# Performance work log

Hardware: AMD Instinct MI355X
Metric: run time of the kernel (lower is better)

Reference implementation:

```python
import jax, jax.numpy as jnp
from jax import lax
import numpy as np


def _conv(x, w):
    # x: [B,Cin,H,W], w: [Cout,Cin,kh,kw] -> [B,Cout,H,W], SAME padding
    return lax.conv_general_dilated(x, w, (1, 1), 'SAME')


def setup_inputs() -> dict:
    key = jax.random.key(0)
    ks = jax.random.split(key, 16)
    B, Hh, W = 8, 256, 256
    inputs = jax.random.normal(ks[0], (B, Hh, W), jnp.float32)
    H0 = jax.random.normal(ks[1], (B, Hh, W), jnp.float32)
    C0 = jax.random.normal(ks[2], (B, 2, Hh, W), jnp.float32)
    # learned scalars: c2 ~ U(0,1), sf ~ N(0, 0.01) shifted away from 0 (it is a divisor)
    c2 = jax.random.uniform(ks[3], (1,), jnp.float32, 0.0, 1.0)
    sf = 0.01 * jax.random.normal(ks[4], (1,), jnp.float32) + 0.02
    # RedNet (assumed small conv encoder-decoder): 1->32->64->32->1, 3x3 SAME, ReLU
    w1 = 0.1 * jax.random.normal(ks[5], (32, 1, 3, 3), jnp.float32)
    b1 = jnp.zeros((32,), jnp.float32)
    w2 = 0.1 * jax.random.normal(ks[6], (64, 32, 3, 3), jnp.float32)
    b2 = jnp.zeros((64,), jnp.float32)
    w3 = 0.1 * jax.random.normal(ks[7], (32, 64, 3, 3), jnp.float32)
    b3 = jnp.zeros((32,), jnp.float32)
    w4 = 0.1 * jax.random.normal(ks[8], (1, 32, 3, 3), jnp.float32)
    b4 = jnp.zeros((1,), jnp.float32)
    return dict(inputs=inputs, H0=H0, C0=C0, c2=c2, sf=sf,
                w1=w1, b1=b1, w2=w2, b2=b2, w3=w3, b3=b3, w4=w4, b4=b4)


def reference(inputs, H0, C0, c2, sf, w1, b1, w2, b2, w3, b3, w4, b4):
    # Fixed 5-point Laplacian stencil (non-trainable in the original module)
    lap_k = jnp.array([[0., 1., 0.], [1., -4., 1.], [0., 1., 0.]],
                      dtype=inputs.dtype)[None, None]  # [1,1,3,3]

    # torch chain: C' = permute/matmul(Wcc^T)/permute + wcu*U
    #   reduces exactly to: C'[:,0] = inputs, C'[:,1] = C_old[:,0]
    C_new = jnp.stack([inputs, C0[:, 0]], axis=1)  # [B,2,H,W]

    V = inputs - H0  # [B,H,W]

    # H = whc . C' = 2*C'[:,0] - C'[:,1] = 2*inputs - C_old[:,0]
    lap = _conv(inputs[:, None], lap_k)[:, 0]  # [B,H,W]
    H = 2.0 * inputs - C0[:, 0] + c2 * lap

    # RedNet on scaled residual V
    h = (V / sf)[:, None]  # [B,1,H,W]
    h = jax.nn.relu(_conv(h, w1) + b1[None, :, None, None])
    h = jax.nn.relu(_conv(h, w2) + b2[None, :, None, None])
    h = jax.nn.relu(_conv(h, w3) + b3[None, :, None, None])
    V_hat = (_conv(h, w4) + b4[None, :, None, None])[:, 0] * sf  # [B,H,W]

    outputs = H + V_hat
    return (outputs, H, C_new, V, V_hat)
```

## Files before the change

kernel.cpp:

```cpp
#include <hip/hip_runtime.h>

#define PLANE 65536
#define WIDTH 256
#define PADW 258
#define PADPLANE 66564

typedef __bf16 v8bf __attribute__((ext_vector_type(8)));
typedef float  v4f  __attribute__((ext_vector_type(4)));

typedef const __attribute__((address_space(1))) unsigned int* gas_ptr;
typedef __attribute__((address_space(3))) unsigned int* las_ptr;

__device__ __forceinline__ void gl_lds(const void* g, void* l) {
  __builtin_amdgcn_global_load_lds((gas_ptr)g, (las_ptr)l, 16, 0, 0);
}

__device__ __forceinline__ int swz(int c) {
  return (c & ~7) | ((c & 7) ^ ((c >> 3) & 7));
}

__device__ __forceinline__ unsigned int pack2(float a, float b) {
  __bf16 ba = (__bf16)a, bb = (__bf16)b;
  unsigned short sa = __builtin_bit_cast(unsigned short, ba);
  unsigned short sb = __builtin_bit_cast(unsigned short, bb);
  return (unsigned int)sa | ((unsigned int)sb << 16);
}

#define WT_N 37440
#define ZR_N (8 * 1028 * 64)
__global__ __launch_bounds__(256) void wz_k(
    const float* __restrict__ w1, const float* __restrict__ w2,
    const float* __restrict__ w3, const float* __restrict__ w4,
    float* __restrict__ w1t, __bf16* __restrict__ B2t,
    __bf16* __restrict__ B3t, float* __restrict__ w4t,
    __bf16* __restrict__ a1, __bf16* __restrict__ a2,
    __bf16* __restrict__ a3)
{
  int t = blockIdx.x * 256 + threadIdx.x;
  if (t < WT_N) {
    if (t < 288) {
      int tap = t >> 5, cout = t & 31;
      w1t[t] = w1[cout * 9 + tap];
    }
    int t2 = t - 288;
    if (t2 >= 0 && t2 < 18432) {
      int cout = t2 / 288, k = t2 % 288;
      int tap = k / 32, cin = k % 32;
      B2t[t2] = (__bf16)w2[cout * 288 + cin * 9 + tap];
    }
    int t3 = t - (288 + 18432);
    if (t3 >= 0 && t3 < 18432) {
      int cout = t3 / 576, k = t3 % 576;
      int tap = k / 64, cin = k % 64;
      B3t[t3] = (__bf16)w3[cout * 576 + cin * 9 + tap];
    }
    int t4 = t - (288 + 18432 + 18432);
    if (t4 >= 0 && t4 < 288) {
      int tap = t4 >> 5, cin = t4 & 31;
      w4t[t4] = w4[cin * 9 + tap];
    }
    return;
  }
  int idx = t - WT_N;
  if (idx >= ZR_N) return;
  unsigned int* p; int C2;
  const int R1 = 8 * 1028 * 16, R2 = 8 * 1028 * 32;
  if (idx < R1)           { p = (unsigned int*)a1; C2 = 16; }
  else if (idx < R1 + R2) { p = (unsigned int*)a2; C2 = 32; idx -= R1; }
  else                    { p = (unsigned int*)a3; C2 = 16; idx -= R1 + R2; }
  int ch = idx % C2;
  int pr = idx / C2;
  int b = pr / 1028, r = pr % 1028;
  int y, x;
  if      (r < 258) { y = 0;           x = r; }
  else if (r < 516) { y = 257;         x = r - 258; }
  else if (r < 772) { y = r - 516 + 1; x = 0; }
  else              { y = r - 772 + 1; x = 257; }
  p[((size_t)b * PADPLANE + y * PADW + x) * C2 + ch] = 0;
}

__global__ __launch_bounds__(256) void prepconv1_k(
    const float* __restrict__ inputs, const float* __restrict__ H0,
    const float* __restrict__ C0, const float* __restrict__ c2p,
    const float* __restrict__ sfp, const float* __restrict__ w1t,
    const float* __restrict__ b1, float* __restrict__ dout,
    __bf16* __restrict__ act1)
{
  const int x = threadIdx.x, y = blockIdx.x, b = blockIdx.y;
  const int p = b * PLANE + y * WIDTH + x;
  const float c2 = c2p[0], sf = sfp[0], rsf = 1.0f / sf;

  float iv[3][3], hv[3][3];
  #pragma unroll
  for (int dy = 0; dy < 3; dy++) {
    int yy = y + dy - 1;
    #pragma unroll
    for (int dx = 0; dx < 3; dx++) {
      int xx = x + dx - 1;
      bool ok = (yy >= 0 && yy < 256 && xx >= 0 && xx < 256);
      int pn = p + (dy - 1) * WIDTH + (dx - 1);
      iv[dy][dx] = ok ? inputs[pn] : 0.f;
      hv[dy][dx] = ok ? H0[pn]     : 0.f;
    }
  }
  const float in = iv[1][1], h0 = hv[1][1];
  const float c0a = C0[b * 131072 + y * WIDTH + x];
  float lap = iv[0][1] + iv[2][1] + iv[1][0] + iv[1][2] - 4.f * in;
  float Hv = 2.f * in - c0a + c2 * lap;
  float V  = in - h0;
  dout[524288 + p]  = Hv;
  dout[2097152 + p] = V;
  dout[1048576 + b * 131072 + y * WIDTH + x]         = in;
  dout[1048576 + b * 131072 + 65536 + y * WIDTH + x] = c0a;

  float acc[32];
  #pragma unroll
  for (int i = 0; i < 32; i++) acc[i] = b1[i];
  #pragma unroll
  for (int tap = 0; tap < 9; tap++) {
    float v = (iv[tap / 3][tap % 3] - hv[tap / 3][tap % 3]) * rsf;
    const float* wp = w1t + tap * 32;
    #pragma unroll
    for (int i = 0; i < 32; i++) acc[i] = fmaf(wp[i], v, acc[i]);
  }
  unsigned int u[16];
  #pragma unroll
  for (int j = 0; j < 16; j++)
    u[j] = pack2(fmaxf(acc[2*j], 0.f), fmaxf(acc[2*j+1], 0.f));
  size_t pa = ((size_t)b * PADPLANE + (y+1) * PADW + (x+1)) * 32;
  uint4* op = reinterpret_cast<uint4*>(act1 + pa);
  #pragma unroll
  for (int j = 0; j < 4; j++)
    op[j] = make_uint4(u[4*j], u[4*j+1], u[4*j+2], u[4*j+3]);
}

#define C2ROWB 8320
template<int ROWS>
__global__ __launch_bounds__(256, 2) void conv2_k(
    const __bf16* __restrict__ in, const __bf16* __restrict__ Bt,
    const float* __restrict__ bias, __bf16* __restrict__ out)
{
  const int lane = threadIdx.x & 63, wave = threadIdx.x >> 6;
  const int l15 = lane & 15, q = lane >> 4;
  const int y0 = blockIdx.x * ROWS, xt = blockIdx.y, b = blockIdx.z;
  const int x0 = xt * 128;
  __shared__ __align__(16) char smem[3 * C2ROWB];
  const __bf16* plane = in + (size_t)b * PADPLANE * 32;

  auto stage = [&](int pr, char* lrow) {
    const char* g = (const char*)(plane + ((size_t)pr * PADW + x0) * 32);
    const int base = wave * 130;
    #pragma unroll
    for (int j = 0; j < 2; j++) {
      int c = base + j * 64 + lane;
      gl_lds(g + (size_t)swz(c) * 16, lrow + (base + j * 64) * 16);
    }
    if (lane < 2) {
      int c = base + 128 + lane;
      gl_lds(g + (size_t)swz(c) * 16, lrow + (base + 128) * 16);
    }
  };

  v8bf breg[9][4];
  #pragma unroll
  for (int tap = 0; tap < 9; tap++)
    #pragma unroll
    for (int nt = 0; nt < 4; nt++)
      breg[tap][nt] = *(const v8bf*)(Bt + (size_t)(nt * 16 + l15) * 288
                                        + tap * 32 + q * 8);
  float bv[4];
  #pragma unroll
  for (int nt = 0; nt < 4; nt++) bv[nt] = bias[nt * 16 + l15];

  #pragma unroll
  for (int r = 0; r < 3; r++) stage(y0 + r, smem + r * C2ROWB);
  __syncthreads();

  for (int i = 0; i < ROWS; i++) {
    v4f acc[2][4];
    #pragma unroll
    for (int mt = 0; mt < 2; mt++)
      #pragma unroll
      for (int nt = 0; nt < 4; nt++)
        acc[mt][nt] = (v4f){bv[nt], bv[nt], bv[nt], bv[nt]};

    #pragma unroll
    for (int tap = 0; tap < 9; tap++) {
      const int dy = tap / 3, dx = tap % 3;
      const char* srow = smem + ((i + dy) % 3) * C2ROWB;
      v8bf af[2];
      #pragma unroll
      for (int mt = 0; mt < 2; mt++) {
        int P = wave * 32 + mt * 16 + l15 + dx;
        af[mt] = *(const v8bf*)(srow + (size_t)swz(P * 4 + q) * 16);
      }
      #pragma unroll
      for (int mt = 0; mt < 2; mt++)
        #pragma unroll
        for (int nt = 0; nt < 4; nt++)
          acc[mt][nt] = __builtin_amdgcn_mfma_f32_16x16x32_bf16(
              af[mt], breg[tap][nt], acc[mt][nt], 0, 0, 0);
    }
    {
      size_t rb = ((size_t)b * PADPLANE + (size_t)(y0 + i + 1) * PADW
                   + x0 + 1) * 64;
      #pragma unroll
      for (int mt = 0; mt < 2; mt++) {
        #pragma unroll
        for (int r = 0; r < 4; r++) {
          size_t pa = rb + (size_t)(wave * 32 + mt * 16 + q * 4 + r) * 64;
          #pragma unroll
          for (int nt = 0; nt < 4; nt++)
            out[pa + nt * 16 + l15] = (__bf16)fmaxf(acc[mt][nt][r], 0.f);
        }
      }
    }
    __syncthreads();
    if (i + 3 < ROWS + 2)
      stage(y0 + i + 3, smem + (i % 3) * C2ROWB);
    __syncthreads();
  }
}

#define C3ROWB 16640
template<int ROWS>
__global__ __launch_bounds__(256, 2) void conv3_k(
    const __bf16* __restrict__ in, const __bf16* __restrict__ Bt,
    const float* __restrict__ bias, __bf16* __restrict__ out)
{
  const int lane = threadIdx.x & 63, wave = threadIdx.x >> 6;
  const int l15 = lane & 15, q = lane >> 4;
  const int y0 = blockIdx.x * ROWS, xt = blockIdx.y, b = blockIdx.z;
  const int x0 = xt * 128;
  __shared__ __align__(16) char smem[4 * C3ROWB];
  const __bf16* plane = in + (size_t)b * PADPLANE * 64;

  auto stage = [&](int pr, char* lrow) {
    const char* g = (const char*)(plane + ((size_t)pr * PADW + x0) * 64);
    const int base = wave * 260;
    #pragma unroll
    for (int j = 0; j < 4; j++) {
      int c = base + j * 64 + lane;
      gl_lds(g + (size_t)swz(c) * 16, lrow + (base + j * 64) * 16);
    }
    if (lane < 4) {
      int c = base + 256 + lane;
      gl_lds(g + (size_t)swz(c) * 16, lrow + (base + 256) * 16);
    }
  };

  v8bf breg[9][2][2];
  #pragma unroll
  for (int tap = 0; tap < 9; tap++)
    #pragma unroll
    for (int kb = 0; kb < 2; kb++)
      #pragma unroll
      for (int nt = 0; nt < 2; nt++)
        breg[tap][kb][nt] = *(const v8bf*)(Bt + (size_t)(nt * 16 + l15) * 576
                                              + tap * 64 + kb * 32 + q * 8);
  float bv[2] = {bias[l15], bias[16 + l15]};

  #pragma unroll
  for (int r = 0; r < 4; r++) stage(y0 + r, smem + r * C3ROWB);
  __syncthreads();

  for (int ps = 0; ps < ROWS / 2; ps++) {
    v4f acc[2][2][2];
    #pragma unroll
    for (int rr = 0; rr < 2; rr++)
      #pragma unroll
      for (int mt = 0; mt < 2; mt++)
        #pragma unroll
        for (int nt = 0; nt < 2; nt++)
          acc[rr][mt][nt] = (v4f){bv[nt], bv[nt], bv[nt], bv[nt]};

    #pragma unroll
    for (int t = 0; t < 4; t++) {
      const char* srow = smem + ((2 * ps + t) & 3) * C3ROWB;
      #pragma unroll
      for (int dx = 0; dx < 3; dx++) {
        #pragma unroll
        for (int kb = 0; kb < 2; kb++) {
          v8bf af[2];
          #pragma unroll
          for (int mt = 0; mt < 2; mt++) {
            int P = wave * 32 + mt * 16 + l15 + dx;
            af[mt] = *(const v8bf*)(srow + (size_t)swz(P * 8 + kb * 4 + q) * 16);
          }
          #pragma unroll
          for (int mt = 0; mt < 2; mt++)
            #pragma unroll
            for (int nt = 0; nt < 2; nt++) {
              if (t <= 2)
                acc[0][mt][nt] = __builtin_amdgcn_mfma_f32_16x16x32_bf16(
                    af[mt], breg[t * 3 + dx][kb][nt], acc[0][mt][nt], 0, 0, 0);
              if (t >= 1)
                acc[1][mt][nt] = __builtin_amdgcn_mfma_f32_16x16x32_bf16(
                    af[mt], breg[(t - 1) * 3 + dx][kb][nt], acc[1][mt][nt],
                    0, 0, 0);
            }
        }
      }
    }
    {
      #pragma unroll
      for (int rr = 0; rr < 2; rr++) {
        size_t rb = ((size_t)b * PADPLANE
                     + (size_t)(y0 + 2 * ps + rr + 1) * PADW + x0 + 1) * 32;
        #pragma unroll
        for (int mt = 0; mt < 2; mt++) {
          #pragma unroll
          for (int r = 0; r < 4; r++) {
            size_t pa = rb + (size_t)(wave * 32 + mt * 16 + q * 4 + r) * 32;
            #pragma unroll
            for (int nt = 0; nt < 2; nt++)
              out[pa + nt * 16 + l15] = (__bf16)fmaxf(acc[rr][mt][nt][r], 0.f);
          }
        }
      }
    }
    __syncthreads();
    if (ps + 1 < ROWS / 2) {
      stage(y0 + 2 * ps + 4, smem + ((2 * ps) & 3) * C3ROWB);
      stage(y0 + 2 * ps + 5, smem + ((2 * ps + 1) & 3) * C3ROWB);
    }
    __syncthreads();
  }
}

__global__ __launch_bounds__(256) void conv4_k(
    const __bf16* __restrict__ act3, const float* __restrict__ w4t,
    const float* __restrict__ b4, const float* __restrict__ sfp,
    float* __restrict__ dout)
{
  const int x = threadIdx.x, y0 = blockIdx.x * 2, b = blockIdx.y;
  const float b4v = b4[0], sf = sfp[0];
  const uint4* base = (const uint4*)(act3 + (size_t)b * PADPLANE * 32);
  float acc0 = b4v, acc1 = b4v;

  #pragma unroll
  for (int t = 0; t < 4; t++) {
    const uint4* rp = base + ((size_t)(y0 + t) * PADW + x) * 4;
    uint4 L[12];
    #pragma unroll
    for (int j = 0; j < 12; j++) L[j] = rp[j];
    #pragma unroll
    for (int j = 0; j < 12; j++) {
      const int dx = j >> 2, c0 = (j & 3) * 8;
      unsigned int uu[4] = {L[j].x, L[j].y, L[j].z, L[j].w};
      float f[8];
      #pragma unroll
      for (int k = 0; k < 4; k++) {
        f[2*k]   = __builtin_bit_cast(float, uu[k] << 16);
        f[2*k+1] = __builtin_bit_cast(float, uu[k] & 0xFFFF0000u);
      }
      if (t <= 2) {
        const float* wp = w4t + (t * 3 + dx) * 32 + c0;
        #pragma unroll
        for (int k = 0; k < 8; k++) acc0 = fmaf(wp[k], f[k], acc0);
      }
      if (t >= 1) {
        const float* wp = w4t + ((t - 1) * 3 + dx) * 32 + c0;
        #pragma unroll
        for (int k = 0; k < 8; k++) acc1 = fmaf(wp[k], f[k], acc1);
      }
    }
  }
  size_t p0 = ((size_t)b << 16) + (size_t)y0 * WIDTH + x;
  float vh0 = acc0 * sf, vh1 = acc1 * sf;
  dout[p0]                   = dout[524288 + p0] + vh0;
  dout[2621440 + p0]         = vh0;
  dout[p0 + WIDTH]           = dout[524288 + p0 + WIDTH] + vh1;
  dout[2621440 + p0 + WIDTH] = vh1;
}

extern "C" void kernel_launch(void* const* d_in, const int* in_sizes, int n_in,
                              void* d_out, int out_size, void* d_ws, size_t ws_size,
                              hipStream_t stream) {
  const float* inputs = (const float*)d_in[0];
  const float* H0     = (const float*)d_in[1];
  const float* C0     = (const float*)d_in[2];
  const float* c2     = (const float*)d_in[3];
  const float* sf     = (const float*)d_in[4];
  const float* w1     = (const float*)d_in[5];
  const float* b1     = (const float*)d_in[6];
  const float* w2     = (const float*)d_in[7];
  const float* b2     = (const float*)d_in[8];
  const float* w3     = (const float*)d_in[9];
  const float* b3     = (const float*)d_in[10];
  const float* w4     = (const float*)d_in[11];
  const float* b4     = (const float*)d_in[12];
  float* out = (float*)d_out;
  float* ws  = (float*)d_ws;

  float*  w1t  = ws;
  float*  w4t  = ws + 288;
  __bf16* B2t  = (__bf16*)(ws + 576);
  __bf16* B3t  = (__bf16*)(ws + 9792);
  __bf16* act1 = (__bf16*)(ws + 19008);
  __bf16* act2 = act1 + (size_t)8 * PADPLANE * 32;
  __bf16* act3 = act2 + (size_t)8 * PADPLANE * 64;

  wz_k<<<2203, 256, 0, stream>>>(w1, w2, w3, w4, w1t, B2t, B3t, w4t,
                                 act1, act2, act3);
  prepconv1_k<<<dim3(256, 8), 256, 0, stream>>>(inputs, H0, C0, c2, sf,
                                                w1t, b1, out, act1);
  conv2_k<8><<<dim3(32, 2, 8), 256, 0, stream>>>(act1, B2t, b2, act2);
  conv3_k<8><<<dim3(32, 2, 8), 256, 0, stream>>>(act2, B3t, b3, act3);
  conv4_k<<<dim3(128, 8), 256, 0, stream>>>(act3, w4t, b4, sf, out);
}
```

Measured before the change: 170.6 us.

## Process row pairs in conv2 and transpose MFMA operands for packed stores

conv2 now computes two output rows per pass from a four-row LDS ring, so each loaded A fragment feeds the MFMAs of both output rows. This mirrors the existing conv3 scheme. In both conv2 and conv3 the MFMA operands are swapped so that each lane holds four consecutive output channels. That lets the epilogue pack them into one 8-byte bf16 store instead of scalar 2-byte stores. The cost is more LDS per block and twice the accumulator registers in conv2, which may reduce occupancy.

After: 186.1 us. 9.1% more time.

```diff
diff --git a/kernel.cpp b/kernel.cpp
--- a/kernel.cpp
+++ b/kernel.cpp
@@ -144,7 +144,7 @@
   const int l15 = lane & 15, q = lane >> 4;
   const int y0 = blockIdx.x * ROWS, xt = blockIdx.y, b = blockIdx.z;
   const int x0 = xt * 128;
-  __shared__ __align__(16) char smem[3 * C2ROWB];
+  __shared__ __align__(16) char smem[4 * C2ROWB];
   const __bf16* plane = in + (size_t)b * PADPLANE * 32;
 
   auto stage = [&](int pr, char* lrow) {
@@ -168,56 +168,71 @@
     for (int nt = 0; nt < 4; nt++)
       breg[tap][nt] = *(const v8bf*)(Bt + (size_t)(nt * 16 + l15) * 288
                                         + tap * 32 + q * 8);
-  float bv[4];
-  #pragma unroll
-  for (int nt = 0; nt < 4; nt++) bv[nt] = bias[nt * 16 + l15];
-
-  #pragma unroll
-  for (int r = 0; r < 3; r++) stage(y0 + r, smem + r * C2ROWB);
+  v4f bv[4];
+  #pragma unroll
+  for (int nt = 0; nt < 4; nt++) bv[nt] = *(const v4f*)(bias + nt * 16 + q * 4);
+
+  #pragma unroll
+  for (int r = 0; r < 4; r++) stage(y0 + r, smem + (r & 3) * C2ROWB);
   __syncthreads();
 
-  for (int i = 0; i < ROWS; i++) {
-    v4f acc[2][4];
-    #pragma unroll
-    for (int mt = 0; mt < 2; mt++)
-      #pragma unroll
-      for (int nt = 0; nt < 4; nt++)
-        acc[mt][nt] = (v4f){bv[nt], bv[nt], bv[nt], bv[nt]};
-
-    #pragma unroll
-    for (int tap = 0; tap < 9; tap++) {
-      const int dy = tap / 3, dx = tap % 3;
-      const char* srow = smem + ((i + dy) % 3) * C2ROWB;
-      v8bf af[2];
+  for (int ps = 0; ps < ROWS / 2; ps++) {
+    v4f acc[2][2][4];
+    #pragma unroll
+    for (int rr = 0; rr < 2; rr++)
+      #pragma unroll
+      for (int mt = 0; mt < 2; mt++)
+        #pragma unroll
+        for (int nt = 0; nt < 4; nt++)
+          acc[rr][mt][nt] = bv[nt];
+
+    #pragma unroll
+    for (int t = 0; t < 4; t++) {
+      const char* srow = smem + ((2 * ps + t) & 3) * C2ROWB;
+      #pragma unroll
+      for (int dx = 0; dx < 3; dx++) {
+        v8bf af[2];
+        #pragma unroll
+        for (int mt = 0; mt < 2; mt++) {
+          int P = wave * 32 + mt * 16 + l15 + dx;
+          af[mt] = *(const v8bf*)(srow + (size_t)swz(P * 4 + q) * 16);
+        }
+        #pragma unroll
+        for (int mt = 0; mt < 2; mt++)
+          #pragma unroll
+          for (int nt = 0; nt < 4; nt++) {
+            if (t <= 2)
+              acc[0][mt][nt] = __builtin_amdgcn_mfma_f32_16x16x32_bf16(
+                  breg[t * 3 + dx][nt], af[mt], acc[0][mt][nt], 0, 0, 0);
+            if (t >= 1)
+              acc[1][mt][nt] = __builtin_amdgcn_mfma_f32_16x16x32_bf16(
+                  breg[(t - 1) * 3 + dx][nt], af[mt], acc[1][mt][nt], 0, 0, 0);
+          }
+      }
+    }
+    #pragma unroll
+    for (int rr = 0; rr < 2; rr++) {
+      size_t rb = ((size_t)b * PADPLANE
+                   + (size_t)(y0 + 2 * ps + rr + 1) * PADW + x0 + 1) * 64;
       #pragma unroll
       for (int mt = 0; mt < 2; mt++) {
-        int P = wave * 32 + mt * 16 + l15 + dx;
-        af[mt] = *(const v8bf*)(srow + (size_t)swz(P * 4 + q) * 16);
-      }
-      #pragma unroll
-      for (int mt = 0; mt < 2; mt++)
-        #pragma unroll
-        for (int nt = 0; nt < 4; nt++)
-          acc[mt][nt] = __builtin_amdgcn_mfma_f32_16x16x32_bf16(
-              af[mt], breg[tap][nt], acc[mt][nt], 0, 0, 0);
-    }
-    {
-      size_t rb = ((size_t)b * PADPLANE + (size_t)(y0 + i + 1) * PADW
-                   + x0 + 1) * 64;
-      #pragma unroll
-      for (int mt = 0; mt < 2; mt++) {
-        #pragma unroll
-        for (int r = 0; r < 4; r++) {
-          size_t pa = rb + (size_t)(wave * 32 + mt * 16 + q * 4 + r) * 64;
-          #pragma unroll
-          for (int nt = 0; nt < 4; nt++)
-            out[pa + nt * 16 + l15] = (__bf16)fmaxf(acc[mt][nt][r], 0.f);
+        size_t pa = rb + (size_t)(wave * 32 + mt * 16 + l15) * 64;
+        #pragma unroll
+        for (int nt = 0; nt < 4; nt++) {
+          float r0 = fmaxf(acc[rr][mt][nt][0], 0.f);
+          float r1 = fmaxf(acc[rr][mt][nt][1], 0.f);
+          float r2 = fmaxf(acc[rr][mt][nt][2], 0.f);
+          float r3 = fmaxf(acc[rr][mt][nt][3], 0.f);
+          *(uint2*)(out + pa + nt * 16 + q * 4) =
+              make_uint2(pack2(r0, r1), pack2(r2, r3));
         }
       }
     }
     __syncthreads();
-    if (i + 3 < ROWS + 2)
-      stage(y0 + i + 3, smem + (i % 3) * C2ROWB);
+    if (ps + 1 < ROWS / 2) {
+      stage(y0 + 2 * ps + 4, smem + ((2 * ps) & 3) * C2ROWB);
+      stage(y0 + 2 * ps + 5, smem + ((2 * ps + 1) & 3) * C2ROWB);
+    }
     __syncthreads();
   }
 }
@@ -258,7 +273,9 @@
       for (int nt = 0; nt < 2; nt++)
         breg[tap][kb][nt] = *(const v8bf*)(Bt + (size_t)(nt * 16 + l15) * 576
                                               + tap * 64 + kb * 32 + q * 8);
-  float bv[2] = {bias[l15], bias[16 + l15]};
+  v4f bv[2];
+  #pragma unroll
+  for (int nt = 0; nt < 2; nt++) bv[nt] = *(const v4f*)(bias + nt * 16 + q * 4);
 
   #pragma unroll
   for (int r = 0; r < 4; r++) stage(y0 + r, smem + r * C3ROWB);
@@ -272,7 +289,7 @@
       for (int mt = 0; mt < 2; mt++)
         #pragma unroll
         for (int nt = 0; nt < 2; nt++)
-          acc[rr][mt][nt] = (v4f){bv[nt], bv[nt], bv[nt], bv[nt]};
+          acc[rr][mt][nt] = bv[nt];
 
     #pragma unroll
     for (int t = 0; t < 4; t++) {
@@ -293,29 +310,30 @@
             for (int nt = 0; nt < 2; nt++) {
               if (t <= 2)
                 acc[0][mt][nt] = __builtin_amdgcn_mfma_f32_16x16x32_bf16(
-                    af[mt], breg[t * 3 + dx][kb][nt], acc[0][mt][nt], 0, 0, 0);
+                    breg[t * 3 + dx][kb][nt], af[mt], acc[0][mt][nt], 0, 0, 0);
               if (t >= 1)
                 acc[1][mt][nt] = __builtin_amdgcn_mfma_f32_16x16x32_bf16(
-                    af[mt], breg[(t - 1) * 3 + dx][kb][nt], acc[1][mt][nt],
+                    breg[(t - 1) * 3 + dx][kb][nt], af[mt], acc[1][mt][nt],
                     0, 0, 0);
             }
         }
       }
     }
-    {
-      #pragma unroll
-      for (int rr = 0; rr < 2; rr++) {
-        size_t rb = ((size_t)b * PADPLANE
-                     + (size_t)(y0 + 2 * ps + rr + 1) * PADW + x0 + 1) * 32;
-        #pragma unroll
-        for (int mt = 0; mt < 2; mt++) {
-          #pragma unroll
-          for (int r = 0; r < 4; r++) {
-            size_t pa = rb + (size_t)(wave * 32 + mt * 16 + q * 4 + r) * 32;
-            #pragma unroll
-            for (int nt = 0; nt < 2; nt++)
-              out[pa + nt * 16 + l15] = (__bf16)fmaxf(acc[rr][mt][nt][r], 0.f);
-          }
+    #pragma unroll
+    for (int rr = 0; rr < 2; rr++) {
+      size_t rb = ((size_t)b * PADPLANE
+                   + (size_t)(y0 + 2 * ps + rr + 1) * PADW + x0 + 1) * 32;
+      #pragma unroll
+      for (int mt = 0; mt < 2; mt++) {
+        size_t pa = rb + (size_t)(wave * 32 + mt * 16 + l15) * 32;
+        #pragma unroll
+        for (int nt = 0; nt < 2; nt++) {
+          float r0 = fmaxf(acc[rr][mt][nt][0], 0.f);
+          float r1 = fmaxf(acc[rr][mt][nt][1], 0.f);
+          float r2 = fmaxf(acc[rr][mt][nt][2], 0.f);
+          float r3 = fmaxf(acc[rr][mt][nt][3], 0.f);
+          *(uint2*)(out + pa + nt * 16 + q * 4) =
+              make_uint2(pack2(r0, r1), pack2(r2, r3));
         }
       }
     }
```
